# Optimization experiments

Hardware: AMD Instinct MI355X
Metric: run time of the kernel (lower is better)

The kernel has to match this reference:

```python
import jax, jax.numpy as jnp
import numpy as np

N_EMBED = 8192
EMBED_DIM = 4
BETA = 0.25


def setup_inputs() -> dict:
    key = jax.random.key(0)
    k1, k2 = jax.random.split(key)
    z = jax.random.normal(k1, (8, EMBED_DIM, 64, 64), dtype=jnp.float32)
    # torch init: uniform(-1/n_embed, 1/n_embed)
    embed_w = jax.random.uniform(k2, (N_EMBED, EMBED_DIM), dtype=jnp.float32,
                                 minval=-1.0 / N_EMBED, maxval=1.0 / N_EMBED)
    return {"z": z, "embed_w": embed_w}


def reference(z, embed_w):
    # z: [B, C, H, W] -> [B, H, W, C]
    z_nhwc = jnp.transpose(z, (0, 2, 3, 1))
    z_flat = z_nhwc.reshape(-1, EMBED_DIM)  # [N, D]
    # squared L2 distances: ||z||^2 + ||e||^2 - 2 z e^T  -> [N, n_embed]
    d = (jnp.sum(z_flat * z_flat, axis=1, keepdims=True)
         + jnp.sum(embed_w * embed_w, axis=1)
         - 2.0 * z_flat @ embed_w.T)
    min_idx = jnp.argmin(d, axis=1)  # [N] int
    z_q = embed_w[min_idx].reshape(z_nhwc.shape)  # [B, H, W, C]
    sg = jax.lax.stop_gradient
    loss = (jnp.mean((sg(z_q) - z_nhwc) ** 2)
            + BETA * jnp.mean((z_q - sg(z_nhwc)) ** 2))
    # straight-through estimator
    z_q_ste = z_nhwc + sg(z_q - z_nhwc)
    z_q_out = jnp.transpose(z_q_ste, (0, 3, 1, 2))  # back to [B, C, H, W]
    return z_q_out, loss, min_idx
```

## Files before the change

### kernel.cpp

```cpp
#include <hip/hip_runtime.h>
#include <math.h>

typedef float v2f __attribute__((ext_vector_type(2)));

#define N_POINTS 32768
#define NUM_EMBED 8192
#define NPAIRS 4096
#define CH 64
#define CPC (NUM_EMBED / CH)
#define PAIRS (NPAIRS / CH)
#define PPT 8
#define RB 512
#define CSTRIDE 4096

__global__ void vq_prep_kernel(const float4* __restrict__ E, v2f* __restrict__ Epk) {
    int p = blockIdx.x * 256 + threadIdx.x;
    if (p < NPAIRS) {
        float4 a = E[2 * p];
        float4 b = E[2 * p + 1];
        Epk[4 * p + 0] = (v2f){a.x, b.x};
        Epk[4 * p + 1] = (v2f){a.y, b.y};
        Epk[4 * p + 2] = (v2f){a.z, b.z};
        Epk[4 * p + 3] = (v2f){a.w, b.w};
    }
}

__device__ __forceinline__ v2f pk_mul(v2f a, v2f b) {
    v2f d; asm("v_pk_mul_f32 %0, %1, %2" : "=v"(d) : "v"(a), "v"(b)); return d;
}
__device__ __forceinline__ v2f pk_fma(v2f a, v2f b, v2f c) {
    v2f d; asm("v_pk_fma_f32 %0, %1, %2, %3" : "=v"(d) : "v"(a), "v"(b), "v"(c)); return d;
}

__device__ __forceinline__ unsigned int fkey(float f) {
    unsigned int b = __float_as_uint(f);
    return b ^ (0x80000000u | (unsigned int)((int)b >> 31));
}

__global__ __launch_bounds__(256) void vq_filter_kernel(
        const float* __restrict__ z, const v2f* __restrict__ Epk,
        float* __restrict__ cmax) {
    __shared__ alignas(16) v2f sE[PAIRS * 4];

    const int c = blockIdx.y;
    if (threadIdx.x < PAIRS * 2) {
        ((float4*)sE)[threadIdx.x] =
            ((const float4*)(Epk + (size_t)c * PAIRS * 4))[threadIdx.x];
    }

    const int n0 = blockIdx.x * (256 * PPT) + threadIdx.x;

    v2f zv[PPT][4];
    #pragma unroll
    for (int p = 0; p < PPT; ++p) {
        int n = n0 + p * 256;
        int b = n >> 12, hw = n & 4095;
        const float* zp = z + b * 16384 + hw;
        zv[p][0] = (v2f){zp[0], zp[0]};
        zv[p][1] = (v2f){zp[CSTRIDE], zp[CSTRIDE]};
        zv[p][2] = (v2f){zp[2 * CSTRIDE], zp[2 * CSTRIDE]};
        zv[p][3] = (v2f){zp[3 * CSTRIDE], zp[3 * CSTRIDE]};
    }

    __syncthreads();

    float run[PPT];
    #pragma unroll
    for (int p = 0; p < PPT; ++p) run[p] = -__builtin_inff();

    const float4* sE4 = (const float4*)sE;
    #pragma unroll 2
    for (int t = 0; t < PAIRS; ++t) {
        float4 E01 = sE4[2 * t];
        float4 E23 = sE4[2 * t + 1];
        v2f e0 = {E01.x, E01.y};
        v2f e1 = {E01.z, E01.w};
        v2f e2 = {E23.x, E23.y};
        v2f e3 = {E23.z, E23.w};
        #pragma unroll
        for (int p = 0; p < PPT; ++p) {
            v2f dot = pk_mul(zv[p][0], e0);
            dot = pk_fma(zv[p][1], e1, dot);
            dot = pk_fma(zv[p][2], e2, dot);
            dot = pk_fma(zv[p][3], e3, dot);
            run[p] = fmaxf(fmaxf(dot.x, dot.y), run[p]);
        }
    }

    #pragma unroll
    for (int p = 0; p < PPT; ++p)
        cmax[(size_t)c * N_POINTS + n0 + p * 256] = run[p];
}

__global__ __launch_bounds__(RB) void vq_resolve_kernel(
        const float* __restrict__ z, const float4* __restrict__ E,
        const float* __restrict__ cmax,
        float* __restrict__ out, double* __restrict__ partial) {
    __shared__ float sCm[CH][9];
    __shared__ double sdata[RB / 64];
    const int lane = threadIdx.x & 63;
    const int wid = threadIdx.x >> 6;
    const int n0 = blockIdx.x * (RB / 64);
    const int n = n0 + wid;

    {
        int t = threadIdx.x;
        int c = t >> 3, i = t & 7;
        sCm[c][i] = cmax[(size_t)c * N_POINTS + n0 + i];
    }

    const int b = n >> 12;
    const int hw = n & 4095;
    const float* zp = z + b * 16384 + hw;
    float z0 = zp[0];
    float z1 = zp[CSTRIDE];
    float z2 = zp[2 * CSTRIDE];
    float z3 = zp[3 * CSTRIDE];
    float zz = __fmul_rn(z0, z0);
    zz = __fadd_rn(zz, __fmul_rn(z1, z1));
    zz = __fadd_rn(zz, __fmul_rn(z2, z2));
    zz = __fadd_rn(zz, __fmul_rn(z3, z3));

    __syncthreads();

    float cm = sCm[lane][wid];
    float gmax = cm;
    #pragma unroll
    for (int off = 32; off; off >>= 1)
        gmax = fmaxf(gmax, __shfl_xor(gmax, off));

    float u = __fmul_rn(__fadd_rn(zz, 0.01f), 2.38418579e-07f);
    float thr = __fsub_rn(gmax, __fadd_rn(__fadd_rn(u, u), 1e-7f));
    unsigned long long mask = __ballot(cm >= thr);

    unsigned long long bkey = ~0ull;
    while (mask) {
        int c = __builtin_ctzll(mask);
        mask &= mask - 1ull;
        int j0 = c * CPC + lane;
        #pragma unroll
        for (int h = 0; h < 2; ++h) {
            int j = j0 + h * 64;
            float4 e = E[j];
            float ee = __fmul_rn(e.x, e.x);
            ee = __fadd_rn(ee, __fmul_rn(e.y, e.y));
            ee = __fadd_rn(ee, __fmul_rn(e.z, e.z));
            ee = __fadd_rn(ee, __fmul_rn(e.w, e.w));
            float dot = __fmul_rn(z0, e.x);
            dot = __fmaf_rn(z1, e.y, dot);
            dot = __fmaf_rn(z2, e.z, dot);
            dot = __fmaf_rn(z3, e.w, dot);
            float d = __fmaf_rn(-2.0f, dot, __fadd_rn(zz, ee));
            unsigned long long key =
                ((unsigned long long)fkey(d) << 32) | (unsigned int)j;
            bkey = key < bkey ? key : bkey;
        }
    }
    #pragma unroll
    for (int off = 32; off; off >>= 1) {
        unsigned long long o = __shfl_xor(bkey, off);
        bkey = o < bkey ? o : bkey;
    }
    int besti = (int)(unsigned int)(bkey & 0xFFFFFFFFull);

    if (lane == 0) {
        float4 e = E[besti];
        float* op = out + b * 16384 + hw;
        float t0 = __fsub_rn(e.x, z0);
        float t1 = __fsub_rn(e.y, z1);
        float t2 = __fsub_rn(e.z, z2);
        float t3 = __fsub_rn(e.w, z3);
        op[0]           = __fadd_rn(z0, t0);
        op[CSTRIDE]     = __fadd_rn(z1, t1);
        op[2 * CSTRIDE] = __fadd_rn(z2, t2);
        op[3 * CSTRIDE] = __fadd_rn(z3, t3);
        out[131073 + n] = (float)besti;
        double ds = (double)__fmul_rn(t0, t0) + (double)__fmul_rn(t1, t1)
                  + (double)__fmul_rn(t2, t2) + (double)__fmul_rn(t3, t3);
        sdata[wid] = ds;
    }
    __syncthreads();
    if (threadIdx.x == 0) {
        double s = 0.0;
        #pragma unroll
        for (int w = 0; w < RB / 64; ++w) s += sdata[w];
        partial[blockIdx.x] = s;
    }
}

__global__ void vq_loss_kernel(const double* __restrict__ partial, float* __restrict__ out) {
    __shared__ double sdata[256];
    int t = threadIdx.x;
    double s = 0.0;
    for (int i = t; i < 4096; i += 256) s += partial[i];
    sdata[t] = s;
    __syncthreads();
    #pragma unroll
    for (int st = 128; st > 0; st >>= 1) {
        if (t < st) sdata[t] += sdata[t + st];
        __syncthreads();
    }
    if (t == 0) {
        float m = (float)(sdata[0] / 131072.0);
        out[131072] = __fadd_rn(m, __fmul_rn(0.25f, m));
    }
}

extern "C" void kernel_launch(void* const* d_in, const int* in_sizes, int n_in,
                              void* d_out, int out_size, void* d_ws, size_t ws_size,
                              hipStream_t stream) {
    const float* z = (const float*)d_in[0];
    const float4* E = (const float4*)d_in[1];
    float* out = (float*)d_out;

    char* ws = (char*)d_ws;
    v2f* Epk = (v2f*)ws;
    float* cmaxb = (float*)(ws + 131072);
    double* partial = (double*)(ws + 131072 + (size_t)CH * N_POINTS * 4);

    vq_prep_kernel<<<NPAIRS / 256, 256, 0, stream>>>(E, Epk);
    vq_filter_kernel<<<dim3(N_POINTS / (256 * PPT), CH), 256, 0, stream>>>(z, Epk, cmaxb);
    vq_resolve_kernel<<<N_POINTS / (RB / 64), RB, 0, stream>>>(z, E, cmaxb, out, partial);
    vq_loss_kernel<<<1, 256, 0, stream>>>(partial, out);
}
```

Before: 55.90 us.

## Compute exact distances in filter pass and resolve argmin from single winning chunk

The filter kernel now computes the full squared distance (||z||^2 + ||e||^2 - 2 z·e) per chunk with packed FP32 ops, using precomputed codebook norms, and stores each chunk's minimum. The resolve kernel picks the first chunk whose minimum equals the global minimum and rescans only that chunk to find the matching index. This drops the threshold-based multi-chunk candidate rescan and the 64-bit key reduction. In exchange the filter inner loop does two more packed ops per pair, and exact-equality matching depends on both kernels computing identical floating-point results.

Result: slower. 63.95 us (+14.4%).

```diff
diff --git a/kernel.cpp b/kernel.cpp
--- a/kernel.cpp
+++ b/kernel.cpp
@@ -13,7 +13,8 @@
 #define RB 512
 #define CSTRIDE 4096
 
-__global__ void vq_prep_kernel(const float4* __restrict__ E, v2f* __restrict__ Epk) {
+__global__ void vq_prep_kernel(const float4* __restrict__ E,
+                               v2f* __restrict__ Epk, v2f* __restrict__ eev) {
     int p = blockIdx.x * 256 + threadIdx.x;
     if (p < NPAIRS) {
         float4 a = E[2 * p];
@@ -22,9 +23,21 @@
         Epk[4 * p + 1] = (v2f){a.y, b.y};
         Epk[4 * p + 2] = (v2f){a.z, b.z};
         Epk[4 * p + 3] = (v2f){a.w, b.w};
-    }
-}
-
+        float ea = __fmul_rn(a.x, a.x);
+        ea = __fadd_rn(ea, __fmul_rn(a.y, a.y));
+        ea = __fadd_rn(ea, __fmul_rn(a.z, a.z));
+        ea = __fadd_rn(ea, __fmul_rn(a.w, a.w));
+        float eb = __fmul_rn(b.x, b.x);
+        eb = __fadd_rn(eb, __fmul_rn(b.y, b.y));
+        eb = __fadd_rn(eb, __fmul_rn(b.z, b.z));
+        eb = __fadd_rn(eb, __fmul_rn(b.w, b.w));
+        eev[p] = (v2f){ea, eb};
+    }
+}
+
+__device__ __forceinline__ v2f pk_add(v2f a, v2f b) {
+    v2f d; asm("v_pk_add_f32 %0, %1, %2" : "=v"(d) : "v"(a), "v"(b)); return d;
+}
 __device__ __forceinline__ v2f pk_mul(v2f a, v2f b) {
     v2f d; asm("v_pk_mul_f32 %0, %1, %2" : "=v"(d) : "v"(a), "v"(b)); return d;
 }
@@ -32,69 +45,79 @@
     v2f d; asm("v_pk_fma_f32 %0, %1, %2, %3" : "=v"(d) : "v"(a), "v"(b), "v"(c)); return d;
 }
 
-__device__ __forceinline__ unsigned int fkey(float f) {
-    unsigned int b = __float_as_uint(f);
-    return b ^ (0x80000000u | (unsigned int)((int)b >> 31));
-}
-
-__global__ __launch_bounds__(256) void vq_filter_kernel(
+__global__ __launch_bounds__(256, 1) void vq_filter_kernel(
         const float* __restrict__ z, const v2f* __restrict__ Epk,
-        float* __restrict__ cmax) {
+        const v2f* __restrict__ eev, float* __restrict__ dmin) {
     __shared__ alignas(16) v2f sE[PAIRS * 4];
+    __shared__ alignas(16) v2f see[PAIRS];
 
     const int c = blockIdx.y;
-    if (threadIdx.x < PAIRS * 2) {
-        ((float4*)sE)[threadIdx.x] =
-            ((const float4*)(Epk + (size_t)c * PAIRS * 4))[threadIdx.x];
+    {
+        const float4* gE = (const float4*)(Epk + (size_t)c * PAIRS * 4);
+        if (threadIdx.x < PAIRS * 2) {
+            ((float4*)sE)[threadIdx.x] = gE[threadIdx.x];
+        } else if (threadIdx.x < PAIRS * 2 + PAIRS / 2) {
+            ((float4*)see)[threadIdx.x - PAIRS * 2] =
+                ((const float4*)(eev + (size_t)c * PAIRS))[threadIdx.x - PAIRS * 2];
+        }
     }
 
     const int n0 = blockIdx.x * (256 * PPT) + threadIdx.x;
 
-    v2f zv[PPT][4];
+    v2f zv[PPT][4], zzv[PPT];
     #pragma unroll
     for (int p = 0; p < PPT; ++p) {
         int n = n0 + p * 256;
         int b = n >> 12, hw = n & 4095;
         const float* zp = z + b * 16384 + hw;
-        zv[p][0] = (v2f){zp[0], zp[0]};
-        zv[p][1] = (v2f){zp[CSTRIDE], zp[CSTRIDE]};
-        zv[p][2] = (v2f){zp[2 * CSTRIDE], zp[2 * CSTRIDE]};
-        zv[p][3] = (v2f){zp[3 * CSTRIDE], zp[3 * CSTRIDE]};
-    }
+        float a0 = zp[0], a1 = zp[CSTRIDE], a2 = zp[2 * CSTRIDE], a3 = zp[3 * CSTRIDE];
+        float zz = __fmul_rn(a0, a0);
+        zz = __fadd_rn(zz, __fmul_rn(a1, a1));
+        zz = __fadd_rn(zz, __fmul_rn(a2, a2));
+        zz = __fadd_rn(zz, __fmul_rn(a3, a3));
+        zv[p][0] = (v2f){a0, a0}; zv[p][1] = (v2f){a1, a1};
+        zv[p][2] = (v2f){a2, a2}; zv[p][3] = (v2f){a3, a3};
+        zzv[p] = (v2f){zz, zz};
+    }
+    const v2f m2v = {-2.0f, -2.0f};
 
     __syncthreads();
 
     float run[PPT];
     #pragma unroll
-    for (int p = 0; p < PPT; ++p) run[p] = -__builtin_inff();
+    for (int p = 0; p < PPT; ++p) run[p] = __builtin_inff();
 
     const float4* sE4 = (const float4*)sE;
-    #pragma unroll 2
+    #pragma unroll 4
     for (int t = 0; t < PAIRS; ++t) {
         float4 E01 = sE4[2 * t];
         float4 E23 = sE4[2 * t + 1];
+        v2f ee2 = see[t];
         v2f e0 = {E01.x, E01.y};
         v2f e1 = {E01.z, E01.w};
         v2f e2 = {E23.x, E23.y};
         v2f e3 = {E23.z, E23.w};
         #pragma unroll
         for (int p = 0; p < PPT; ++p) {
+            v2f szz = pk_add(zzv[p], ee2);
             v2f dot = pk_mul(zv[p][0], e0);
             dot = pk_fma(zv[p][1], e1, dot);
             dot = pk_fma(zv[p][2], e2, dot);
             dot = pk_fma(zv[p][3], e3, dot);
-            run[p] = fmaxf(fmaxf(dot.x, dot.y), run[p]);
+            v2f d2 = pk_fma(m2v, dot, szz);
+            run[p] = fminf(fminf(d2.x, d2.y), run[p]);
         }
     }
 
     #pragma unroll
     for (int p = 0; p < PPT; ++p)
-        cmax[(size_t)c * N_POINTS + n0 + p * 256] = run[p];
+        dmin[(size_t)c * N_POINTS + n0 + p * 256] = run[p];
 }
 
 __global__ __launch_bounds__(RB) void vq_resolve_kernel(
         const float* __restrict__ z, const float4* __restrict__ E,
-        const float* __restrict__ cmax,
+        const v2f* __restrict__ Epk, const v2f* __restrict__ eev,
+        const float* __restrict__ dmin,
         float* __restrict__ out, double* __restrict__ partial) {
     __shared__ float sCm[CH][9];
     __shared__ double sdata[RB / 64];
@@ -105,8 +128,7 @@
 
     {
         int t = threadIdx.x;
-        int c = t >> 3, i = t & 7;
-        sCm[c][i] = cmax[(size_t)c * N_POINTS + n0 + i];
+        sCm[t >> 3][t & 7] = dmin[(size_t)(t >> 3) * N_POINTS + n0 + (t & 7)];
     }
 
     const int b = n >> 12;
@@ -124,44 +146,37 @@
     __syncthreads();
 
     float cm = sCm[lane][wid];
-    float gmax = cm;
+    float gmin = cm;
     #pragma unroll
     for (int off = 32; off; off >>= 1)
-        gmax = fmaxf(gmax, __shfl_xor(gmax, off));
-
-    float u = __fmul_rn(__fadd_rn(zz, 0.01f), 2.38418579e-07f);
-    float thr = __fsub_rn(gmax, __fadd_rn(__fadd_rn(u, u), 1e-7f));
-    unsigned long long mask = __ballot(cm >= thr);
-
-    unsigned long long bkey = ~0ull;
-    while (mask) {
-        int c = __builtin_ctzll(mask);
-        mask &= mask - 1ull;
-        int j0 = c * CPC + lane;
-        #pragma unroll
-        for (int h = 0; h < 2; ++h) {
-            int j = j0 + h * 64;
-            float4 e = E[j];
-            float ee = __fmul_rn(e.x, e.x);
-            ee = __fadd_rn(ee, __fmul_rn(e.y, e.y));
-            ee = __fadd_rn(ee, __fmul_rn(e.z, e.z));
-            ee = __fadd_rn(ee, __fmul_rn(e.w, e.w));
-            float dot = __fmul_rn(z0, e.x);
-            dot = __fmaf_rn(z1, e.y, dot);
-            dot = __fmaf_rn(z2, e.z, dot);
-            dot = __fmaf_rn(z3, e.w, dot);
-            float d = __fmaf_rn(-2.0f, dot, __fadd_rn(zz, ee));
-            unsigned long long key =
-                ((unsigned long long)fkey(d) << 32) | (unsigned int)j;
-            bkey = key < bkey ? key : bkey;
-        }
-    }
+        gmin = fminf(gmin, __shfl_xor(gmin, off));
+
+    unsigned long long mask = __ballot(cm == gmin);
+    int cstar = __builtin_ctzll(mask);
+
+    int p = cstar * PAIRS + lane;
+    const v2f* ep = Epk + (size_t)p * 4;
+    v2f e0 = ep[0], e1 = ep[1], e2 = ep[2], e3 = ep[3];
+    v2f ee2 = eev[p];
+    v2f z0v = {z0, z0}, z1v = {z1, z1}, z2v = {z2, z2}, z3v = {z3, z3};
+    v2f zzv = {zz, zz};
+    v2f m2v = {-2.0f, -2.0f};
+    v2f szz = pk_add(zzv, ee2);
+    v2f dot = pk_mul(z0v, e0);
+    dot = pk_fma(z1v, e1, dot);
+    dot = pk_fma(z2v, e2, dot);
+    dot = pk_fma(z3v, e3, dot);
+    v2f d2 = pk_fma(m2v, dot, szz);
+
+    int cand = 0x7FFFFFFF;
+    if (d2.y == gmin) cand = 2 * p + 1;
+    if (d2.x == gmin) cand = 2 * p;
     #pragma unroll
     for (int off = 32; off; off >>= 1) {
-        unsigned long long o = __shfl_xor(bkey, off);
-        bkey = o < bkey ? o : bkey;
-    }
-    int besti = (int)(unsigned int)(bkey & 0xFFFFFFFFull);
+        int o = __shfl_xor(cand, off);
+        cand = o < cand ? o : cand;
+    }
+    int besti = cand;
 
     if (lane == 0) {
         float4 e = E[besti];
@@ -215,11 +230,12 @@
 
     char* ws = (char*)d_ws;
     v2f* Epk = (v2f*)ws;
-    float* cmaxb = (float*)(ws + 131072);
-    double* partial = (double*)(ws + 131072 + (size_t)CH * N_POINTS * 4);
-
-    vq_prep_kernel<<<NPAIRS / 256, 256, 0, stream>>>(E, Epk);
-    vq_filter_kernel<<<dim3(N_POINTS / (256 * PPT), CH), 256, 0, stream>>>(z, Epk, cmaxb);
-    vq_resolve_kernel<<<N_POINTS / (RB / 64), RB, 0, stream>>>(z, E, cmaxb, out, partial);
+    v2f* eev = (v2f*)(ws + 131072);
+    float* dminb = (float*)(ws + 163840);
+    double* partial = (double*)(ws + 163840 + (size_t)CH * N_POINTS * 4);
+
+    vq_prep_kernel<<<NPAIRS / 256, 256, 0, stream>>>(E, Epk, eev);
+    vq_filter_kernel<<<dim3(N_POINTS / (256 * PPT), CH), 256, 0, stream>>>(z, Epk, eev, dminb);
+    vq_resolve_kernel<<<N_POINTS / (RB / 64), RB, 0, stream>>>(z, E, Epk, eev, dminb, out, partial);
     vq_loss_kernel<<<1, 256, 0, stream>>>(partial, out);
 }
```
